# Kernel tuning notes

Hardware: AMD Instinct MI355X
Metric: run time of the kernel (lower is better)

Reference implementation:

```python
import jax, jax.numpy as jnp
import numpy as np

D_MODEL = 1024

def setup_inputs() -> dict:
    key = jax.random.key(0)
    ks = jax.random.split(key, 5)
    d = D_MODEL
    s = 1.0 / np.sqrt(d)
    x = jax.random.normal(ks[0], (4, 4096, d), dtype=jnp.float32)
    qkv_w = jax.random.normal(ks[1], (3 * d, d), dtype=jnp.float32) * s
    qkv_b = jax.random.normal(ks[2], (3 * d,), dtype=jnp.float32) * 0.01
    out_w = jax.random.normal(ks[3], (d, d), dtype=jnp.float32) * s
    out_b = jax.random.normal(ks[4], (d,), dtype=jnp.float32) * 0.01
    return {"x": x, "qkv_w": qkv_w, "qkv_b": qkv_b, "out_w": out_w, "out_b": out_b}

def reference(x, qkv_w, qkv_b, out_w, out_b):
    # x: [b, s, d]; Linear applies x @ W^T + b (torch convention)
    d_model = x.shape[-1]
    qkv = jnp.einsum('bsd,ed->bse', x, qkv_w) + qkv_b  # [b, s, 3d]
    q, k, v = jnp.split(qkv, 3, axis=-1)
    # full-attention branch (chunk_size is None): scores scaled by 1/sqrt(d_model)
    scores = jnp.einsum('bqd,bkd->bqk', q, k) / jnp.sqrt(jnp.float32(d_model))
    attn = jax.nn.softmax(scores, axis=-1)
    attn_out = jnp.einsum('bqk,bkd->bqd', attn, v)
    return jnp.einsum('bsd,ed->bse', attn_out, out_w) + out_b
```

## Files before the change

kernel.cpp:

```cpp
#include <hip/hip_runtime.h>
#include <hip/hip_bf16.h>

typedef __bf16 bf16x8 __attribute__((ext_vector_type(8)));
typedef float f32x4 __attribute__((ext_vector_type(4)));
typedef _Float16 h8 __attribute__((ext_vector_type(8)));
typedef unsigned short u16x8 __attribute__((ext_vector_type(8)));

__device__ inline unsigned short f2b(float x) {
    __hip_bfloat16 h = __float2bfloat16(x);
    return __builtin_bit_cast(unsigned short, h);
}

__device__ inline void gload16(const void* g, void* l) {
    __builtin_amdgcn_global_load_lds(
        (const __attribute__((address_space(1))) unsigned int*)g,
        (__attribute__((address_space(3))) unsigned int*)l, 16, 0, 0);
}

#define BAR  asm volatile("s_barrier" ::: "memory")
#define VMC(N) asm volatile("s_waitcnt vmcnt(" #N ")" ::: "memory")

#define RD_A(BASE, MO)                                                \
    af[0][0] = *(const bf16x8*)((BASE) + (MO) * 1024 + aoff0);        \
    af[0][1] = *(const bf16x8*)((BASE) + (MO) * 1024 + aoff1);        \
    af[1][0] = *(const bf16x8*)((BASE) + ((MO) + 1) * 1024 + aoff0);  \
    af[1][1] = *(const bf16x8*)((BASE) + ((MO) + 1) * 1024 + aoff1);

#define RD_B(BASE)                                                    \
    _Pragma("unroll")                                                 \
    for (int n_ = 0; n_ < 4; ++n_) {                                  \
        bfr[n_][0] = *(const bf16x8*)((BASE) + n_ * 1024 + aoff0);    \
        bfr[n_][1] = *(const bf16x8*)((BASE) + n_ * 1024 + aoff1);    \
    }

#define MFMA_Q(MO)                                                    \
    __builtin_amdgcn_s_setprio(1);                                    \
    _Pragma("unroll")                                                 \
    for (int kk_ = 0; kk_ < 2; ++kk_)                                 \
        _Pragma("unroll")                                             \
        for (int mi_ = 0; mi_ < 2; ++mi_)                             \
            _Pragma("unroll")                                         \
            for (int n_ = 0; n_ < 4; ++n_)                            \
                acc[(MO) + mi_][n_] =                                 \
                    __builtin_amdgcn_mfma_f32_16x16x32_bf16(          \
                        af[mi_][kk_], bfr[n_][kk_],                   \
                        acc[(MO) + mi_][n_], 0, 0, 0);                \
    __builtin_amdgcn_s_setprio(0);

template<int EPI, int SWZ>
__global__ __launch_bounds__(512, 2) void gemm_nt(
    const unsigned short* __restrict__ A, const unsigned short* __restrict__ B,
    long aZ, long bZ, int lda, int ldb, int K,
    const float* __restrict__ bias,
    void* __restrict__ C0, void* __restrict__ C1, void* __restrict__ C2,
    long cZ, int ldc, float scale, int gx, int gy)
{
    __shared__ __attribute__((aligned(16))) unsigned short lds[2][4][8192];

    int wgid;
    if (SWZ) {
        const int nwg = (int)gridDim.x;
        const int bid = (int)blockIdx.x;
        const int qch = nwg >> 3, rch = nwg & 7;
        const int xcd = bid & 7, idx = bid >> 3;
        wgid = (xcd < rch ? xcd * (qch + 1)
                          : rch * (qch + 1) + (xcd - rch) * qch) + idx;
    } else {
        wgid = (int)blockIdx.x;
    }
    const int bx = wgid % gx;
    const int rem = wgid / gx;
    const int by = rem % gy;
    const int z = rem / gy;

    const int t = threadIdx.x;
    const int lane = t & 63, wid = t >> 6;
    const int wr = wid >> 2, wc = wid & 3;
    const int tileM = by * 256, tileN = bx * 256;
    A += (size_t)z * aZ;
    B += (size_t)z * bZ;

    f32x4 acc[8][4] = {};

    const int l4 = lane & 15, qw = lane >> 4, sw = lane & 7;
    const int aoff0 = l4 * 64 + ((qw ^ sw) << 3);
    const int aoff1 = l4 * 64 + (((4 | qw) ^ sw) << 3);

    const unsigned short* aB0 = &lds[0][wr][0];
    const unsigned short* aB1 = &lds[1][wr][0];
    const unsigned short* bB0 = &lds[0][2 + (wc >> 1)][0] + (wc & 1) * 4096;
    const unsigned short* bB1 = &lds[1][2 + (wc >> 1)][0] + (wc & 1) * 4096;

    char* const ldsA[2] = {(char*)&lds[0][0][0], (char*)&lds[1][0][0]};
    char* const ldsB[2] = {(char*)&lds[0][2][0], (char*)&lds[1][2][0]};

    const int srow = t >> 3;
    const int sg = ((t ^ (t >> 3)) & 7) << 3;
    const unsigned short* Asrc0 = A + (size_t)(tileM + srow) * lda + sg;
    const unsigned short* Asrc1 = Asrc0 + (size_t)128 * lda;
    const unsigned short* Bsrc0 = B + (size_t)(tileN + srow) * ldb + sg;
    const unsigned short* Bsrc1 = Bsrc0 + (size_t)128 * ldb;

    auto stageA = [&](char* Lb, int koff, int h) {
        char* dst = Lb + h * 16384 + wid * 1024;
        const unsigned short* s = (h ? Asrc1 : Asrc0) + koff;
        gload16(s, dst);
        gload16(s + (size_t)64 * lda, dst + 8192);
    };
    auto stageB = [&](char* Lb, int koff, int h) {
        char* dst = Lb + h * 16384 + wid * 1024;
        const unsigned short* s = (h ? Bsrc1 : Bsrc0) + koff;
        gload16(s, dst);
        gload16(s + (size_t)64 * ldb, dst + 8192);
    };

    const int NT = K >> 6;
    const int NI = NT >> 1;

    stageA(ldsA[0], 0, 0); stageA(ldsA[0], 0, 1);
    stageB(ldsB[0], 0, 0); stageB(ldsB[0], 0, 1);
    stageB(ldsB[1], 64, 0); stageB(ldsB[1], 64, 1);
    VMC(4);
    BAR;

    bf16x8 af[2][2], bfr[4][2];

#pragma unroll 1
    for (int i = 0; i < NI - 1; ++i) {
        const int kb = i * 128;
        const int ko = kb + 64, ke2 = kb + 128, ko2 = kb + 192;

        RD_B(bB0); RD_A(aB0, 0);
        BAR; stageA(ldsA[1], ko, 0);
        MFMA_Q(0)
        RD_A(aB0, 2);
        BAR; stageA(ldsA[1], ko, 1);
        MFMA_Q(2)
        RD_A(aB0, 4);
        BAR; stageB(ldsB[0], ke2, 0);
        MFMA_Q(4)
        RD_A(aB0, 6);
        VMC(2);
        BAR; stageB(ldsB[0], ke2, 1);
        MFMA_Q(6)
        RD_B(bB1); RD_A(aB1, 0);
        BAR; stageA(ldsA[0], ke2, 0);
        MFMA_Q(0)
        RD_A(aB1, 2);
        BAR; stageA(ldsA[0], ke2, 1);
        MFMA_Q(2)
        RD_A(aB1, 4);
        BAR; stageB(ldsB[1], ko2, 0);
        MFMA_Q(4)
        RD_A(aB1, 6);
        VMC(2);
        BAR; stageB(ldsB[1], ko2, 1);
        MFMA_Q(6)
    }

    {
        const int ko = (NI - 1) * 128 + 64;
        RD_B(bB0); RD_A(aB0, 0);
        BAR; stageA(ldsA[1], ko, 0);
        MFMA_Q(0)
        RD_A(aB0, 2);
        BAR; stageA(ldsA[1], ko, 1);
        MFMA_Q(2)
        RD_A(aB0, 4);
        BAR;
        MFMA_Q(4)
        RD_A(aB0, 6);
        VMC(0);
        BAR;
        MFMA_Q(6)
        RD_B(bB1); RD_A(aB1, 0);
        BAR;
        MFMA_Q(0)
        RD_A(aB1, 2);
        BAR;
        MFMA_Q(2)
        RD_A(aB1, 4);
        BAR;
        MFMA_Q(4)
        RD_A(aB1, 6);
        BAR;
        MFMA_Q(6)
    }

    const int lr = lane >> 4, lc = lane & 15;
#pragma unroll
    for (int m = 0; m < 8; ++m) {
#pragma unroll
        for (int n = 0; n < 4; ++n) {
            f32x4 v = acc[m][n];
            const int col = tileN + wc * 64 + n * 16 + lc;
            const int row0 = tileM + wr * 128 + m * 16 + lr * 4;
            if (EPI == 0) {
                const float bv = bias[col];
                if (col < 2048) {
                    unsigned short* dst = (col < 1024) ? (unsigned short*)C0
                                                       : (unsigned short*)C1;
                    const int cc = col & 1023;
#pragma unroll
                    for (int j = 0; j < 4; ++j)
                        dst[(size_t)(row0 + j) * 1024 + cc] = f2b(v[j] + bv);
                } else {
                    const int b = row0 >> 12, s = row0 & 4095;
                    ushort4 h4;
                    h4.x = f2b(v[0] + bv); h4.y = f2b(v[1] + bv);
                    h4.z = f2b(v[2] + bv); h4.w = f2b(v[3] + bv);
                    *(ushort4*)((unsigned short*)C2 +
                                ((size_t)b * 1024 + (col - 2048)) * 4096 + s) = h4;
                }
            } else if (EPI == 1) {
#pragma unroll
                for (int j = 0; j < 4; ++j)
                    ((_Float16*)C0)[(size_t)z * cZ + (size_t)(row0 + j) * ldc + col] =
                        (_Float16)(v[j] * scale);
            } else if (EPI == 2) {
#pragma unroll
                for (int j = 0; j < 4; ++j)
                    ((unsigned short*)C0)[(size_t)z * cZ + (size_t)(row0 + j) * ldc + col] =
                        f2b(v[j]);
            } else {
#pragma unroll
                for (int j = 0; j < 4; ++j)
                    ((float*)C0)[(size_t)(row0 + j) * ldc + col] = v[j] + bias[col];
            }
        }
    }
}

__global__ __launch_bounds__(256) void softmax_rows(unsigned short* __restrict__ sc)
{
    const size_t rowoff = (size_t)blockIdx.x * 4096;
    const int t = threadIdx.x;

    h8 a = *(const h8*)(sc + rowoff + t * 8);
    h8 b = *(const h8*)(sc + rowoff + 2048 + t * 8);
    float v[16];
#pragma unroll
    for (int i = 0; i < 8; ++i) { v[i] = (float)a[i]; v[8 + i] = (float)b[i]; }

    float mx = -1e30f;
#pragma unroll
    for (int i = 0; i < 16; ++i) mx = fmaxf(mx, v[i]);
#pragma unroll
    for (int o = 32; o > 0; o >>= 1) mx = fmaxf(mx, __shfl_xor(mx, o));
    __shared__ float redm[4];
    if ((t & 63) == 0) redm[t >> 6] = mx;
    __syncthreads();
    mx = fmaxf(fmaxf(redm[0], redm[1]), fmaxf(redm[2], redm[3]));

    float sum = 0.f;
#pragma unroll
    for (int i = 0; i < 16; ++i) { v[i] = expf(v[i] - mx); sum += v[i]; }
#pragma unroll
    for (int o = 32; o > 0; o >>= 1) sum += __shfl_xor(sum, o);
    __shared__ float reds[4];
    if ((t & 63) == 0) reds[t >> 6] = sum;
    __syncthreads();
    sum = reds[0] + reds[1] + reds[2] + reds[3];
    const float rs = 1.f / sum;

    u16x8 w0, w1;
#pragma unroll
    for (int i = 0; i < 8; ++i) {
        w0[i] = f2b(v[i] * rs);
        w1[i] = f2b(v[8 + i] * rs);
    }
    *(u16x8*)(sc + rowoff + t * 8) = w0;
    *(u16x8*)(sc + rowoff + 2048 + t * 8) = w1;
}

__global__ __launch_bounds__(256) void cast_bf16(
    const float* __restrict__ in, unsigned short* __restrict__ out, int n4)
{
    const int i = blockIdx.x * 256 + threadIdx.x;
    if (i < n4) {
        float4 f = ((const float4*)in)[i];
        ushort4 o;
        o.x = f2b(f.x); o.y = f2b(f.y); o.z = f2b(f.z); o.w = f2b(f.w);
        ((ushort4*)out)[i] = o;
    }
}

extern "C" void kernel_launch(void* const* d_in, const int* in_sizes, int n_in,
                              void* d_out, int out_size, void* d_ws, size_t ws_size,
                              hipStream_t stream)
{
    const float* x      = (const float*)d_in[0];
    const float* qkv_w  = (const float*)d_in[1];
    const float* qkv_b  = (const float*)d_in[2];
    const float* out_w  = (const float*)d_in[3];
    const float* out_b  = (const float*)d_in[4];
    float* out = (float*)d_out;

    unsigned short* W = (unsigned short*)d_ws;
    const size_t M16 = 16777216;

    if (ws_size >= 236978176ull) {
        unsigned short* sc   = W;
        unsigned short* q    = sc + 67108864;
        unsigned short* kk   = q + M16;
        unsigned short* vT   = kk + M16;
        unsigned short* wo   = vT + M16;
        unsigned short* xb   = sc;
        unsigned short* wqkv = sc + M16;
        unsigned short* ao   = q;

        cast_bf16<<<16384, 256, 0, stream>>>(x, xb, 4194304);
        cast_bf16<<<3072, 256, 0, stream>>>(qkv_w, wqkv, 786432);
        cast_bf16<<<1024, 256, 0, stream>>>(out_w, wo, 262144);

        gemm_nt<0, 0><<<12 * 64, 512, 0, stream>>>(
            xb, wqkv, 0, 0, 1024, 1024, 1024, qkv_b, q, kk, vT, 0, 0, 0.f, 12, 64);

        gemm_nt<1, 0><<<16 * 16 * 4, 512, 0, stream>>>(
            q, kk, 4194304, 4194304, 1024, 1024, 1024, nullptr,
            sc, nullptr, nullptr, 16777216, 4096, 0.03125f, 16, 16);

        softmax_rows<<<16384, 256, 0, stream>>>(sc);

        gemm_nt<2, 1><<<4 * 16 * 4, 512, 0, stream>>>(
            sc, vT, 16777216, 4194304, 4096, 4096, 4096, nullptr,
            ao, nullptr, nullptr, 4194304, 1024, 0.f, 4, 16);

        gemm_nt<3, 0><<<4 * 64, 512, 0, stream>>>(
            ao, wo, 0, 0, 1024, 1024, 1024, out_b,
            out, nullptr, nullptr, 0, 1024, 0.f, 4, 64);
    } else {
        unsigned short* sc   = W;
        unsigned short* q    = sc + M16;
        unsigned short* kk   = q + M16;
        unsigned short* vT   = kk + M16;
        unsigned short* ao   = vT + M16;
        unsigned short* wo   = ao + M16;
        unsigned short* wqkv = wo + 1048576;
        unsigned short* xb   = sc;

        cast_bf16<<<16384, 256, 0, stream>>>(x, xb, 4194304);
        cast_bf16<<<3072, 256, 0, stream>>>(qkv_w, wqkv, 786432);
        cast_bf16<<<1024, 256, 0, stream>>>(out_w, wo, 262144);

        gemm_nt<0, 0><<<12 * 64, 512, 0, stream>>>(
            xb, wqkv, 0, 0, 1024, 1024, 1024, qkv_b, q, kk, vT, 0, 0, 0.f, 12, 64);

        for (int z = 0; z < 4; ++z) {
            const size_t zo = (size_t)z * 4194304;
            gemm_nt<1, 0><<<16 * 16, 512, 0, stream>>>(
                q + zo, kk + zo, 0, 0, 1024, 1024, 1024, nullptr,
                sc, nullptr, nullptr, 0, 4096, 0.03125f, 16, 16);
            softmax_rows<<<4096, 256, 0, stream>>>(sc);
            gemm_nt<2, 1><<<4 * 16, 512, 0, stream>>>(
                sc, vT + zo, 0, 0, 4096, 4096, 4096, nullptr,
                ao + zo, nullptr, nullptr, 0, 1024, 0.f, 4, 16);
        }

        gemm_nt<3, 0><<<4 * 64, 512, 0, stream>>>(
            ao, wo, 0, 0, 1024, 1024, 1024, out_b,
            out, nullptr, nullptr, 0, 1024, 0.f, 4, 64);
    }
}
```

Before: 442.4 us.

## Add 16-wave GEMM variant for attention score and PV matmuls

Introduces gemm_nt16, a 1024-thread (16-wave) version of the 256x256 tile GEMM. Each wave computes a 64x64 subtile with a finer-grained interleave of LDS reads, global-to-LDS staging and MFMAs, and it is used for the QK^T and softmax*V GEMMs. The aim is more waves per CU to hide latency, and fewer accumulators per wave to cut register pressure. It costs more barriers per k-step, and each wave now re-reads the shared B fragments from LDS. Softmax also switches from expf to the faster, less accurate __expf.

```diff
diff --git a/kernel.cpp b/kernel.cpp
--- a/kernel.cpp
+++ b/kernel.cpp
@@ -19,6 +19,7 @@
 
 #define BAR  asm volatile("s_barrier" ::: "memory")
 #define VMC(N) asm volatile("s_waitcnt vmcnt(" #N ")" ::: "memory")
+
 
 #define RD_A(BASE, MO)                                                \
     af[0][0] = *(const bf16x8*)((BASE) + (MO) * 1024 + aoff0);        \
@@ -212,20 +213,181 @@
                     *(ushort4*)((unsigned short*)C2 +
                                 ((size_t)b * 1024 + (col - 2048)) * 4096 + s) = h4;
                 }
-            } else if (EPI == 1) {
+            } else {
+#pragma unroll
+                for (int j = 0; j < 4; ++j)
+                    ((float*)C0)[(size_t)(row0 + j) * ldc + col] = v[j] + bias[col];
+            }
+        }
+    }
+}
+
+
+#define RD_A16(BASE, MF)                                              \
+    afc[0] = *(const bf16x8*)((BASE) + (MF) * 1024 + aoff0);          \
+    afc[1] = *(const bf16x8*)((BASE) + (MF) * 1024 + aoff1);
+
+#define MFMA_W(MF)                                                    \
+    __builtin_amdgcn_s_setprio(1);                                    \
+    _Pragma("unroll")                                                 \
+    for (int n_ = 0; n_ < 4; ++n_) {                                  \
+        acc[MF][n_] = __builtin_amdgcn_mfma_f32_16x16x32_bf16(        \
+            afc[0], bfr[n_][0], acc[MF][n_], 0, 0, 0);                \
+        acc[MF][n_] = __builtin_amdgcn_mfma_f32_16x16x32_bf16(        \
+            afc[1], bfr[n_][1], acc[MF][n_], 0, 0, 0);                \
+    }                                                                 \
+    __builtin_amdgcn_s_setprio(0);
+
+template<int EPI, int SWZ>
+__global__ __launch_bounds__(1024, 4) void gemm_nt16(
+    const unsigned short* __restrict__ A, const unsigned short* __restrict__ B,
+    long aZ, long bZ, int lda, int ldb, int K,
+    void* __restrict__ C0, long cZ, int ldc, float scale, int gx, int gy)
+{
+    __shared__ __attribute__((aligned(16))) unsigned short lds[2][4][8192];
+
+    int wgid;
+    if (SWZ) {
+        const int nwg = (int)gridDim.x;
+        const int bid = (int)blockIdx.x;
+        const int qch = nwg >> 3, rch = nwg & 7;
+        const int xcd = bid & 7, idx = bid >> 3;
+        wgid = (xcd < rch ? xcd * (qch + 1)
+                          : rch * (qch + 1) + (xcd - rch) * qch) + idx;
+    } else {
+        wgid = (int)blockIdx.x;
+    }
+    const int bx = wgid % gx;
+    const int rem = wgid / gx;
+    const int by = rem % gy;
+    const int z = rem / gy;
+
+    const int t = threadIdx.x;
+    const int lane = t & 63, wid = t >> 6;
+    const int wr = wid >> 2, wc = wid & 3;
+    const int tileM = by * 256, tileN = bx * 256;
+    A += (size_t)z * aZ;
+    B += (size_t)z * bZ;
+
+    f32x4 acc[4][4] = {};
+
+    const int l4 = lane & 15, qw = lane >> 4, sw = lane & 7;
+    const int aoff0 = l4 * 64 + ((qw ^ sw) << 3);
+    const int aoff1 = l4 * 64 + (((4 | qw) ^ sw) << 3);
+
+    const unsigned short* aB0 = &lds[0][wr >> 1][0] + (wr & 1) * 4096;
+    const unsigned short* aB1 = &lds[1][wr >> 1][0] + (wr & 1) * 4096;
+    const unsigned short* bB0 = &lds[0][2 + (wc >> 1)][0] + (wc & 1) * 4096;
+    const unsigned short* bB1 = &lds[1][2 + (wc >> 1)][0] + (wc & 1) * 4096;
+
+    char* const ldsA[2] = {(char*)&lds[0][0][0], (char*)&lds[1][0][0]};
+    char* const ldsB[2] = {(char*)&lds[0][2][0], (char*)&lds[1][2][0]};
+
+    const int srow = t >> 3;
+    const int sg = ((t ^ (t >> 3)) & 7) << 3;
+    const unsigned short* Asrc0 = A + (size_t)(tileM + srow) * lda + sg;
+    const unsigned short* Asrc1 = Asrc0 + (size_t)128 * lda;
+    const unsigned short* Bsrc0 = B + (size_t)(tileN + srow) * ldb + sg;
+    const unsigned short* Bsrc1 = Bsrc0 + (size_t)128 * ldb;
+
+    auto stageA = [&](char* Lb, int koff, int h) {
+        gload16((h ? Asrc1 : Asrc0) + koff, Lb + h * 16384 + t * 16);
+    };
+    auto stageB = [&](char* Lb, int koff, int h) {
+        gload16((h ? Bsrc1 : Bsrc0) + koff, Lb + h * 16384 + t * 16);
+    };
+
+    const int NT = K >> 6;
+    const int NI = NT >> 1;
+
+    stageA(ldsA[0], 0, 0); stageA(ldsA[0], 0, 1);
+    stageB(ldsB[0], 0, 0); stageB(ldsB[0], 0, 1);
+    stageB(ldsB[1], 64, 0); stageB(ldsB[1], 64, 1);
+    VMC(2);
+    BAR;
+
+    bf16x8 afc[2], bfr[4][2];
+
+#pragma unroll 1
+    for (int i = 0; i < NI - 1; ++i) {
+        const int kb = i * 128;
+        const int ko = kb + 64, ke2 = kb + 128, ko2 = kb + 192;
+
+        RD_B(bB0); RD_A16(aB0, 0);
+        BAR; stageA(ldsA[1], ko, 0);
+        MFMA_W(0)
+        RD_A16(aB0, 1);
+        BAR; stageA(ldsA[1], ko, 1);
+        MFMA_W(1)
+        RD_A16(aB0, 2);
+        BAR; stageB(ldsB[0], ke2, 0);
+        MFMA_W(2)
+        RD_A16(aB0, 3);
+        VMC(1);
+        BAR; stageB(ldsB[0], ke2, 1);
+        MFMA_W(3)
+        RD_B(bB1); RD_A16(aB1, 0);
+        BAR; stageA(ldsA[0], ke2, 0);
+        MFMA_W(0)
+        RD_A16(aB1, 1);
+        BAR; stageA(ldsA[0], ke2, 1);
+        MFMA_W(1)
+        RD_A16(aB1, 2);
+        BAR; stageB(ldsB[1], ko2, 0);
+        MFMA_W(2)
+        RD_A16(aB1, 3);
+        VMC(1);
+        BAR; stageB(ldsB[1], ko2, 1);
+        MFMA_W(3)
+    }
+
+    {
+        const int ko = (NI - 1) * 128 + 64;
+        RD_B(bB0); RD_A16(aB0, 0);
+        BAR; stageA(ldsA[1], ko, 0);
+        MFMA_W(0)
+        RD_A16(aB0, 1);
+        BAR; stageA(ldsA[1], ko, 1);
+        MFMA_W(1)
+        RD_A16(aB0, 2);
+        BAR;
+        MFMA_W(2)
+        RD_A16(aB0, 3);
+        VMC(0);
+        BAR;
+        MFMA_W(3)
+        RD_B(bB1); RD_A16(aB1, 0);
+        BAR;
+        MFMA_W(0)
+        RD_A16(aB1, 1);
+        BAR;
+        MFMA_W(1)
+        RD_A16(aB1, 2);
+        BAR;
+        MFMA_W(2)
+        RD_A16(aB1, 3);
+        BAR;
+        MFMA_W(3)
+    }
+
+    const int lr = lane >> 4, lc = lane & 15;
+#pragma unroll
+    for (int m = 0; m < 4; ++m) {
+#pragma unroll
+        for (int n = 0; n < 4; ++n) {
+            f32x4 v = acc[m][n];
+            const int col = tileN + wc * 64 + n * 16 + lc;
+            const int row0 = tileM + wr * 64 + m * 16 + lr * 4;
+            if (EPI == 1) {
 #pragma unroll
                 for (int j = 0; j < 4; ++j)
                     ((_Float16*)C0)[(size_t)z * cZ + (size_t)(row0 + j) * ldc + col] =
                         (_Float16)(v[j] * scale);
-            } else if (EPI == 2) {
+            } else {
 #pragma unroll
                 for (int j = 0; j < 4; ++j)
                     ((unsigned short*)C0)[(size_t)z * cZ + (size_t)(row0 + j) * ldc + col] =
                         f2b(v[j]);
-            } else {
-#pragma unroll
-                for (int j = 0; j < 4; ++j)
-                    ((float*)C0)[(size_t)(row0 + j) * ldc + col] = v[j] + bias[col];
             }
         }
     }
@@ -254,7 +416,7 @@
 
     float sum = 0.f;
 #pragma unroll
-    for (int i = 0; i < 16; ++i) { v[i] = expf(v[i] - mx); sum += v[i]; }
+    for (int i = 0; i < 16; ++i) { v[i] = __expf(v[i] - mx); sum += v[i]; }
 #pragma unroll
     for (int o = 32; o > 0; o >>= 1) sum += __shfl_xor(sum, o);
     __shared__ float reds[4];
@@ -316,15 +478,15 @@
         gemm_nt<0, 0><<<12 * 64, 512, 0, stream>>>(
             xb, wqkv, 0, 0, 1024, 1024, 1024, qkv_b, q, kk, vT, 0, 0, 0.f, 12, 64);
 
-        gemm_nt<1, 0><<<16 * 16 * 4, 512, 0, stream>>>(
-            q, kk, 4194304, 4194304, 1024, 1024, 1024, nullptr,
-            sc, nullptr, nullptr, 16777216, 4096, 0.03125f, 16, 16);
+        gemm_nt16<1, 0><<<16 * 16 * 4, 1024, 0, stream>>>(
+            q, kk, 4194304, 4194304, 1024, 1024, 1024,
+            sc, 16777216, 4096, 0.03125f, 16, 16);
 
         softmax_rows<<<16384, 256, 0, stream>>>(sc);
 
-        gemm_nt<2, 1><<<4 * 16 * 4, 512, 0, stream>>>(
-            sc, vT, 16777216, 4194304, 4096, 4096, 4096, nullptr,
-            ao, nullptr, nullptr, 4194304, 1024, 0.f, 4, 16);
+        gemm_nt16<2, 1><<<4 * 16 * 4, 1024, 0, stream>>>(
+            sc, vT, 16777216, 4194304, 4096, 4096, 4096,
+            ao, 4194304, 1024, 0.f, 4, 16);
 
         gemm_nt<3, 0><<<4 * 64, 512, 0, stream>>>(
             ao, wo, 0, 0, 1024, 1024, 1024, out_b,
@@ -348,13 +510,13 @@
 
         for (int z = 0; z < 4; ++z) {
             const size_t zo = (size_t)z * 4194304;
-            gemm_nt<1, 0><<<16 * 16, 512, 0, stream>>>(
-                q + zo, kk + zo, 0, 0, 1024, 1024, 1024, nullptr,
-                sc, nullptr, nullptr, 0, 4096, 0.03125f, 16, 16);
+            gemm_nt16<1, 0><<<16 * 16, 1024, 0, stream>>>(
+                q + zo, kk + zo, 0, 0, 1024, 1024, 1024,
+                sc, 0, 4096, 0.03125f, 16, 16);
             softmax_rows<<<4096, 256, 0, stream>>>(sc);
-            gemm_nt<2, 1><<<4 * 16, 512, 0, stream>>>(
-                sc, vT + zo, 0, 0, 4096, 4096, 4096, nullptr,
-                ao + zo, nullptr, nullptr, 0, 1024, 0.f, 4, 16);
+            gemm_nt16<2, 1><<<4 * 16, 1024, 0, stream>>>(
+                sc, vT + zo, 0, 0, 4096, 4096, 4096,
+                ao + zo, 0, 1024, 0.f, 4, 16);
         }
 
         gemm_nt<3, 0><<<4 * 64, 512, 0, stream>>>(
```

Result: slower. 717.5 us (+62.2%).
